# Performance work log

Hardware: AMD Instinct MI355X
Metric: run time of the kernel (lower is better)

## Reference

```python
import jax, jax.numpy as jnp
import numpy as np

B, IN_CH, OFF_CH, OUT_CH, H, W, K = 2, 256, 256, 256, 128, 128, 3
KK = K * K


def setup_inputs() -> dict:
    key = jax.random.key(0)
    k0, k1, k2, k3, k4 = jax.random.split(key, 5)
    x = jax.random.normal(k0, (B, IN_CH, H, W), jnp.float32)
    off = jax.random.normal(k1, (B, OFF_CH, H, W), jnp.float32)
    # xavier_uniform-scale (approximated with scaled normals)
    s_off = (2.0 / (OFF_CH + 3 * KK)) ** 0.5
    w_off = jax.random.normal(k2, (3 * KK, OFF_CH, 1, 1), jnp.float32) * s_off
    b_off = jnp.zeros((3 * KK,), jnp.float32)  # init_offset zeros the bias
    s_w = (2.0 / (IN_CH * KK + OUT_CH * KK)) ** 0.5
    w = jax.random.normal(k3, (OUT_CH, IN_CH, K, K), jnp.float32) * s_w
    b = jax.random.normal(k4, (OUT_CH,), jnp.float32) * 0.01
    return {"x": x, "off": off, "w_off": w_off, "b_off": b_off, "w": w, "b": b}


def _bilinear_gather(x, ys, xs):
    # Zero outside the image (per DCNv2 corner validity check).
    Bb, C, Hin, Win = x.shape
    x_flat = x.reshape(Bb, C, Hin * Win)
    y0 = jnp.floor(ys)
    x0 = jnp.floor(xs)
    wy1 = ys - y0
    wx1 = xs - x0
    wy0 = 1.0 - wy1
    wx0 = 1.0 - wx1

    def corner(yc, xc, wgt):
        valid = (yc >= 0) & (yc <= Hin - 1) & (xc >= 0) & (xc <= Win - 1)
        yi = jnp.clip(yc, 0, Hin - 1).astype(jnp.int32)
        xi = jnp.clip(xc, 0, Win - 1).astype(jnp.int32)
        idx = (yi * Win + xi)[:, None, :]  # [B,1,N]
        v = jnp.take_along_axis(x_flat, idx, axis=2)  # [B,C,N]
        return v * (wgt * valid.astype(x.dtype))[:, None, :]

    return (corner(y0, x0, wy0 * wx0) + corner(y0, x0 + 1, wy0 * wx1)
            + corner(y0 + 1, x0, wy1 * wx0) + corner(y0 + 1, x0 + 1, wy1 * wx1))


def reference(x, off, w_off, b_off, w, b):
    Bb, Cin, Hin, Win = x.shape
    pad = K // 2
    # 1x1 offset/mask conv
    out = jnp.einsum('oc,bchw->bohw', w_off[:, :, 0, 0], off) + b_off[None, :, None, None]
    o1, o2, mask = jnp.split(out, 3, axis=1)
    offset = jnp.concatenate([o1, o2], axis=1)  # [B, 2*KK, H, W]
    mask = jax.nn.sigmoid(mask)                 # [B, KK, H, W]
    # DCNv2 reads offset channels interleaved: (dy_k, dx_k) for kernel point k
    offs = offset.reshape(Bb, KK, 2, Hin, Win)
    dy, dx = offs[:, :, 0], offs[:, :, 1]       # [B, KK, H, W]
    kh = (jnp.arange(KK) // K).astype(x.dtype)
    kw = (jnp.arange(KK) % K).astype(x.dtype)
    iy = jnp.arange(Hin, dtype=x.dtype)
    ix = jnp.arange(Win, dtype=x.dtype)
    ys = iy[None, None, :, None] + (kh - pad)[None, :, None, None] + dy
    xs = ix[None, None, None, :] + (kw - pad)[None, :, None, None] + dx
    val = _bilinear_gather(x, ys.reshape(Bb, -1), xs.reshape(Bb, -1))  # [B,C,KK*H*W]
    val = val.reshape(Bb, Cin, KK, Hin, Win) * mask[:, None]
    y = jnp.einsum('ock,bckhw->bohw', w.reshape(w.shape[0], Cin, KK), val)
    y = y + b[None, :, None, None]
    return jax.nn.relu(y)
```

## Files before the change

### kernel.cpp

```cpp
#include <hip/hip_runtime.h>
#include <stdint.h>

#define HH 128
#define WW 128
#define CIN 256
#define OCH 256
#define HW (HH*WW)

typedef __attribute__((ext_vector_type(8))) short bf16x8;
typedef __attribute__((ext_vector_type(16))) float f32x16;

static __device__ __forceinline__ uint16_t f2bf(float f) {
  uint32_t u = __builtin_bit_cast(uint32_t, f);
  u += 0x7FFFu + ((u >> 16) & 1u);
  return (uint16_t)(u >> 16);
}
static __device__ __forceinline__ float bf2f(uint16_t h) {
  uint32_t u = ((uint32_t)h) << 16;
  return __builtin_bit_cast(float, u);
}

__global__ void pack_w_kernel(const float* __restrict__ w, uint16_t* __restrict__ wpk) {
  int i = blockIdx.x * 256 + threadIdx.x;
  int ci = i & 7;
  int oc = (i >> 3) & 255;
  int c8 = (i >> 11) & 31;
  int k  = i >> 16;
  int c = c8 * 8 + ci;
  wpk[i] = f2bf(w[(oc * 256 + c) * 9 + k]);
}

__global__ void transpose_kernel(const float* __restrict__ x, uint32_t* __restrict__ xt) {
  __shared__ float tile[64][65];
  int wg = blockIdx.x;
  int b  = wg >> 10;
  int r  = wg & 1023;
  int pt = r >> 2, ct = r & 3;
  int p0 = pt * 64, c0 = ct * 64;
  int t = threadIdx.x;
#pragma unroll
  for (int i = 0; i < 16; ++i) {
    int cl = i * 4 + (t >> 6);
    tile[cl][t & 63] = x[(size_t)(b * CIN + c0 + cl) * HW + p0 + (t & 63)];
  }
  __syncthreads();
  int c2 = t & 31, pr = t >> 5;
#pragma unroll
  for (int i = 0; i < 8; ++i) {
    int pl = i * 8 + pr;
    uint32_t lo = f2bf(tile[2 * c2][pl]);
    uint32_t hi = f2bf(tile[2 * c2 + 1][pl]);
    xt[(size_t)(b * HW + p0 + pl) * 128 + (c0 >> 1) + c2] = lo | (hi << 16);
  }
}

__global__ void offc_kernel(const float* __restrict__ off, const float* __restrict__ w_off,
                            const float* __restrict__ b_off, float* __restrict__ offs) {
  __shared__ float wl[27 * 256];
  int t = threadIdx.x;
  for (int r = t; r < 27 * 256; r += 64) wl[r] = w_off[r];
  __syncthreads();
  int px = blockIdx.x * 64 + t;
  int b = px >> 14, yx = px & 16383;
  float acc[27];
#pragma unroll
  for (int j = 0; j < 27; ++j) acc[j] = b_off[j];
  const float* op = off + (size_t)b * CIN * HW + yx;
  for (int c = 0; c < 256; c += 4) {
    float v0 = op[(size_t)(c + 0) * HW];
    float v1 = op[(size_t)(c + 1) * HW];
    float v2 = op[(size_t)(c + 2) * HW];
    float v3 = op[(size_t)(c + 3) * HW];
#pragma unroll
    for (int j = 0; j < 27; ++j) {
      acc[j] = fmaf(wl[j * 256 + c + 0], v0, acc[j]);
      acc[j] = fmaf(wl[j * 256 + c + 1], v1, acc[j]);
      acc[j] = fmaf(wl[j * 256 + c + 2], v2, acc[j]);
      acc[j] = fmaf(wl[j * 256 + c + 3], v3, acc[j]);
    }
  }
  float* o = offs + (size_t)px * 27;
#pragma unroll
  for (int k = 0; k < 9; ++k) {
    o[k * 3 + 0] = acc[2 * k];
    o[k * 3 + 1] = acc[2 * k + 1];
    o[k * 3 + 2] = 1.f / (1.f + expf(-acc[18 + k]));
  }
}

__global__ __launch_bounds__(256) void main_kernel(
    const uint32_t* __restrict__ xt, const float* __restrict__ offs,
    const uint16_t* __restrict__ wpk, const float* __restrict__ bias,
    float* __restrict__ out) {
  __shared__ struct __align__(16) { unsigned char A[64 * 512]; float offs_l[64 * 27]; } sm;

  int wg = blockIdx.x;
  wg = (wg & 7) * 64 + (wg >> 3);
  int b = wg >> 8;
  int tile = wg & 255;
  int y0 = (tile >> 3) * 4, x0 = (tile & 7) * 16;

  int tid = threadIdx.x;
  int lane = tid & 63;
  int wv = tid >> 6;
  int l31 = lane & 31, g = lane >> 5;

  {
    int base = b * HW + y0 * WW + x0;
    for (int r = tid; r < 64 * 27; r += 256) {
      int pyl = r / 432;
      int rem = r - pyl * 432;
      sm.offs_l[pyl * 432 + rem] = offs[(size_t)(base + pyl * WW) * 27 + rem];
    }
  }
  f32x16 acc[2][2] = {};
  __syncthreads();

  const int hw = tid >> 5;
  const int j = tid & 31;
  const uint4* xt4 = (const uint4*)xt;
  const uint4* wp4 = (const uint4*)wpk;
  const int pb = b * HW;
  const uint32_t rswz = (uint32_t)((lane & 7) << 4);

#pragma unroll 1
  for (int k = 0; k < 9; ++k) {
    int kh = k / 3 - 1, kw = k % 3 - 1;
#pragma unroll 2
    for (int i = 0; i < 8; ++i) {
      int px = hw * 8 + i;
      int py = px >> 4, pxx = px & 15;
      float dy = sm.offs_l[px * 27 + k * 3 + 0];
      float dx = sm.offs_l[px * 27 + k * 3 + 1];
      float m  = sm.offs_l[px * 27 + k * 3 + 2];
      float ys = (float)(y0 + py + kh) + dy;
      float xs = (float)(x0 + pxx + kw) + dx;
      float yf = floorf(ys), xf = floorf(xs);
      float wy1 = ys - yf, wx1 = xs - xf;
      float wy0 = 1.f - wy1, wx0 = 1.f - wx1;
      int iy0 = (int)yf, ix0 = (int)xf;
      int iy1 = iy0 + 1, ix1 = ix0 + 1;
      float vy0 = (iy0 >= 0 && iy0 < HH) ? 1.f : 0.f;
      float vy1 = (iy1 >= 0 && iy1 < HH) ? 1.f : 0.f;
      float vx0 = (ix0 >= 0 && ix0 < WW) ? 1.f : 0.f;
      float vx1 = (ix1 >= 0 && ix1 < WW) ? 1.f : 0.f;
      float w00 = wy0 * wx0 * vy0 * vx0 * m;
      float w01 = wy0 * wx1 * vy0 * vx1 * m;
      float w10 = wy1 * wx0 * vy1 * vx0 * m;
      float w11 = wy1 * wx1 * vy1 * vx1 * m;
      int cy0 = iy0 < 0 ? 0 : (iy0 > HH - 1 ? HH - 1 : iy0);
      int cy1 = iy1 < 0 ? 0 : (iy1 > HH - 1 ? HH - 1 : iy1);
      int cx0 = ix0 < 0 ? 0 : (ix0 > WW - 1 ? WW - 1 : ix0);
      int cx1 = ix1 < 0 ? 0 : (ix1 > WW - 1 ? WW - 1 : ix1);
      uint4 q00 = xt4[(size_t)(pb + cy0 * WW + cx0) * 32 + j];
      uint4 q01 = xt4[(size_t)(pb + cy0 * WW + cx1) * 32 + j];
      uint4 q10 = xt4[(size_t)(pb + cy1 * WW + cx0) * 32 + j];
      uint4 q11 = xt4[(size_t)(pb + cy1 * WW + cx1) * 32 + j];
      uint32_t u00[4] = {q00.x, q00.y, q00.z, q00.w};
      uint32_t u01[4] = {q01.x, q01.y, q01.z, q01.w};
      uint32_t u10[4] = {q10.x, q10.y, q10.z, q10.w};
      uint32_t u11[4] = {q11.x, q11.y, q11.z, q11.w};
      uint32_t ow[4];
#pragma unroll
      for (int q = 0; q < 4; ++q) {
        float lo = w00 * bf2f((uint16_t)u00[q]) + w01 * bf2f((uint16_t)u01[q])
                 + w10 * bf2f((uint16_t)u10[q]) + w11 * bf2f((uint16_t)u11[q]);
        float hi = w00 * bf2f((uint16_t)(u00[q] >> 16)) + w01 * bf2f((uint16_t)(u01[q] >> 16))
                 + w10 * bf2f((uint16_t)(u10[q] >> 16)) + w11 * bf2f((uint16_t)(u11[q] >> 16));
        ow[q] = (uint32_t)f2bf(lo) | ((uint32_t)f2bf(hi) << 16);
      }
      *(uint4*)(&sm.A[px * 512 + ((j * 16) ^ ((px & 7) << 4))]) =
          make_uint4(ow[0], ow[1], ow[2], ow[3]);
    }
    __syncthreads();

    int oc0 = wv * 64 + l31;
#pragma unroll
    for (int chunk = 0; chunk < 8; ++chunk) {
#pragma unroll
      for (int cs = 0; cs < 2; ++cs) {
        int boff = (chunk * 64 + cs * 32 + g * 16) ^ rswz;
        uint4 ua0 = *(const uint4*)(&sm.A[l31 * 512 + boff]);
        uint4 ua1 = *(const uint4*)(&sm.A[(l31 + 32) * 512 + boff]);
        int bidx = k * 8192 + (chunk * 4 + cs * 2 + g) * 256;
        uint4 ub0 = wp4[bidx + oc0];
        uint4 ub1 = wp4[bidx + oc0 + 32];
        bf16x8 a0 = __builtin_bit_cast(bf16x8, ua0);
        bf16x8 a1 = __builtin_bit_cast(bf16x8, ua1);
        bf16x8 b0 = __builtin_bit_cast(bf16x8, ub0);
        bf16x8 b1 = __builtin_bit_cast(bf16x8, ub1);
        acc[0][0] = __builtin_amdgcn_mfma_f32_32x32x16_bf16(a0, b0, acc[0][0], 0, 0, 0);
        acc[0][1] = __builtin_amdgcn_mfma_f32_32x32x16_bf16(a0, b1, acc[0][1], 0, 0, 0);
        acc[1][0] = __builtin_amdgcn_mfma_f32_32x32x16_bf16(a1, b0, acc[1][0], 0, 0, 0);
        acc[1][1] = __builtin_amdgcn_mfma_f32_32x32x16_bf16(a1, b1, acc[1][1], 0, 0, 0);
      }
    }
    __syncthreads();
  }

  float bias0 = bias[wv * 64 + l31];
  float bias1 = bias[wv * 64 + 32 + l31];
#pragma unroll
  for (int tm = 0; tm < 2; ++tm) {
#pragma unroll
    for (int tn = 0; tn < 2; ++tn) {
      int oc = wv * 64 + tn * 32 + l31;
      float bv = tn ? bias1 : bias0;
#pragma unroll
      for (int r = 0; r < 16; ++r) {
        int row = (r & 3) + 8 * (r >> 2) + 4 * g + 32 * tm;
        int y = y0 + (row >> 4), x = x0 + (row & 15);
        float v = acc[tm][tn][r] + bv;
        out[((size_t)(b * OCH + oc) << 14) + (y << 7) + x] = fmaxf(v, 0.f);
      }
    }
  }
}

extern "C" void kernel_launch(void* const* d_in, const int* in_sizes, int n_in,
                              void* d_out, int out_size, void* d_ws, size_t ws_size,
                              hipStream_t stream) {
  const float* x     = (const float*)d_in[0];
  const float* off   = (const float*)d_in[1];
  const float* w_off = (const float*)d_in[2];
  const float* b_off = (const float*)d_in[3];
  const float* w     = (const float*)d_in[4];
  const float* bias  = (const float*)d_in[5];
  float* out = (float*)d_out;
  char* ws = (char*)d_ws;
  uint32_t* xt   = (uint32_t*)ws;
  float*    offs = (float*)(ws + 16777216);
  uint16_t* wpk  = (uint16_t*)(ws + 16777216 + 3538944);

  pack_w_kernel<<<2304, 256, 0, stream>>>(w, wpk);
  transpose_kernel<<<2048, 256, 0, stream>>>(x, xt);
  offc_kernel<<<512, 64, 0, stream>>>(off, w_off, b_off, offs);
  main_kernel<<<512, 256, 0, stream>>>(xt, offs, wpk, bias, out);
}
```

Baseline: 262.5 us.

## Double-buffer deformable gather with MFMA, shrink tiles, split offset conv channels

The main kernel now uses 32-pixel tiles with double-buffered LDS. Bilinear gathers for the next kernel tap are issued while MFMAs for the current tap run, using setprio and a single lightweight barrier per tap. The offset conv splits its channel reduction across four waves and reduces through LDS with coalesced output writes, and the transpose uses float4 loads. Smaller tiles double the grid and raise occupancy but halve reuse of the weight (B) operand, which now must be re-read from global per tile.

```diff
diff --git a/kernel.cpp b/kernel.cpp
--- a/kernel.cpp
+++ b/kernel.cpp
@@ -19,6 +19,8 @@
   uint32_t u = ((uint32_t)h) << 16;
   return __builtin_bit_cast(float, u);
 }
+
+#define LBAR() asm volatile("s_waitcnt lgkmcnt(0)\ns_barrier" ::: "memory")
 
 __global__ void pack_w_kernel(const float* __restrict__ w, uint16_t* __restrict__ wpk) {
   int i = blockIdx.x * 256 + threadIdx.x;
@@ -38,10 +40,13 @@
   int pt = r >> 2, ct = r & 3;
   int p0 = pt * 64, c0 = ct * 64;
   int t = threadIdx.x;
-#pragma unroll
-  for (int i = 0; i < 16; ++i) {
-    int cl = i * 4 + (t >> 6);
-    tile[cl][t & 63] = x[(size_t)(b * CIN + c0 + cl) * HW + p0 + (t & 63)];
+  int px4 = (t & 15) * 4;
+#pragma unroll
+  for (int i = 0; i < 4; ++i) {
+    int cl = i * 16 + (t >> 4);
+    const float4 v = *(const float4*)&x[(size_t)(b * CIN + c0 + cl) * HW + p0 + px4];
+    tile[cl][px4 + 0] = v.x; tile[cl][px4 + 1] = v.y;
+    tile[cl][px4 + 2] = v.z; tile[cl][px4 + 3] = v.w;
   }
   __syncthreads();
   int c2 = t & 31, pr = t >> 5;
@@ -54,51 +59,75 @@
   }
 }
 
-__global__ void offc_kernel(const float* __restrict__ off, const float* __restrict__ w_off,
-                            const float* __restrict__ b_off, float* __restrict__ offs) {
+__global__ __launch_bounds__(256) void offc_kernel(const float* __restrict__ off,
+                                                   const float* __restrict__ w_off,
+                                                   const float* __restrict__ b_off,
+                                                   float* __restrict__ offs) {
   __shared__ float wl[27 * 256];
+  __shared__ float red[3][64][29];
   int t = threadIdx.x;
-  for (int r = t; r < 27 * 256; r += 64) wl[r] = w_off[r];
-  __syncthreads();
-  int px = blockIdx.x * 64 + t;
+  for (int r = t; r < 27 * 256; r += 256) wl[r] = w_off[r];
+  int pxl = t & 63, q = t >> 6;
+  int px = blockIdx.x * 64 + pxl;
   int b = px >> 14, yx = px & 16383;
   float acc[27];
 #pragma unroll
-  for (int j = 0; j < 27; ++j) acc[j] = b_off[j];
+  for (int jj = 0; jj < 27; ++jj) acc[jj] = 0.f;
   const float* op = off + (size_t)b * CIN * HW + yx;
-  for (int c = 0; c < 256; c += 4) {
-    float v0 = op[(size_t)(c + 0) * HW];
-    float v1 = op[(size_t)(c + 1) * HW];
-    float v2 = op[(size_t)(c + 2) * HW];
-    float v3 = op[(size_t)(c + 3) * HW];
-#pragma unroll
-    for (int j = 0; j < 27; ++j) {
-      acc[j] = fmaf(wl[j * 256 + c + 0], v0, acc[j]);
-      acc[j] = fmaf(wl[j * 256 + c + 1], v1, acc[j]);
-      acc[j] = fmaf(wl[j * 256 + c + 2], v2, acc[j]);
-      acc[j] = fmaf(wl[j * 256 + c + 3], v3, acc[j]);
-    }
-  }
-  float* o = offs + (size_t)px * 27;
-#pragma unroll
-  for (int k = 0; k < 9; ++k) {
-    o[k * 3 + 0] = acc[2 * k];
-    o[k * 3 + 1] = acc[2 * k + 1];
-    o[k * 3 + 2] = 1.f / (1.f + expf(-acc[18 + k]));
-  }
-}
-
-__global__ __launch_bounds__(256) void main_kernel(
+  int cbase = q * 64;
+  __syncthreads();
+  for (int c = 0; c < 64; c += 4) {
+    float v0 = op[(size_t)(cbase + c + 0) * HW];
+    float v1 = op[(size_t)(cbase + c + 1) * HW];
+    float v2 = op[(size_t)(cbase + c + 2) * HW];
+    float v3 = op[(size_t)(cbase + c + 3) * HW];
+    const float* wr = wl + cbase + c;
+#pragma unroll
+    for (int jj = 0; jj < 27; ++jj) {
+      acc[jj] = fmaf(wr[jj * 256 + 0], v0, acc[jj]);
+      acc[jj] = fmaf(wr[jj * 256 + 1], v1, acc[jj]);
+      acc[jj] = fmaf(wr[jj * 256 + 2], v2, acc[jj]);
+      acc[jj] = fmaf(wr[jj * 256 + 3], v3, acc[jj]);
+    }
+  }
+  if (q > 0) {
+#pragma unroll
+    for (int jj = 0; jj < 27; ++jj) red[q - 1][pxl][jj] = acc[jj];
+  }
+  __syncthreads();
+  if (q == 0) {
+    float fin[27];
+#pragma unroll
+    for (int jj = 0; jj < 27; ++jj)
+      acc[jj] += b_off[jj] + red[0][pxl][jj] + red[1][pxl][jj] + red[2][pxl][jj];
+#pragma unroll
+    for (int k = 0; k < 9; ++k) {
+      fin[3 * k + 0] = acc[2 * k];
+      fin[3 * k + 1] = acc[2 * k + 1];
+      fin[3 * k + 2] = 1.f / (1.f + __expf(-acc[18 + k]));
+    }
+#pragma unroll
+    for (int jj = 0; jj < 27; ++jj) red[0][pxl][jj] = fin[jj];
+  }
+  __syncthreads();
+  float* obase = offs + (size_t)blockIdx.x * 64 * 27;
+  for (int r = t; r < 64 * 27; r += 256) {
+    int p = r / 27, e = r - p * 27;
+    obase[r] = red[0][p][e];
+  }
+}
+
+__global__ __launch_bounds__(256, 4) void main_kernel(
     const uint32_t* __restrict__ xt, const float* __restrict__ offs,
     const uint16_t* __restrict__ wpk, const float* __restrict__ bias,
     float* __restrict__ out) {
-  __shared__ struct __align__(16) { unsigned char A[64 * 512]; float offs_l[64 * 27]; } sm;
+  __shared__ struct __align__(16) { unsigned char A[2][32 * 512]; float offs_l[32 * 27]; } sm;
 
   int wg = blockIdx.x;
-  wg = (wg & 7) * 64 + (wg >> 3);
-  int b = wg >> 8;
-  int tile = wg & 255;
-  int y0 = (tile >> 3) * 4, x0 = (tile & 7) * 16;
+  wg = (wg & 7) * 128 + (wg >> 3);
+  int b = wg >> 9;
+  int tile = wg & 511;
+  int y0 = (tile >> 4) * 4, x0 = (tile & 15) * 8;
 
   int tid = threadIdx.x;
   int lane = tid & 63;
@@ -107,112 +136,141 @@
 
   {
     int base = b * HW + y0 * WW + x0;
-    for (int r = tid; r < 64 * 27; r += 256) {
-      int pyl = r / 432;
-      int rem = r - pyl * 432;
-      sm.offs_l[pyl * 432 + rem] = offs[(size_t)(base + pyl * WW) * 27 + rem];
-    }
-  }
-  f32x16 acc[2][2] = {};
-  __syncthreads();
+    for (int r = tid; r < 32 * 27; r += 256) {
+      int pyl = r / 216;
+      int rem = r - pyl * 216;
+      sm.offs_l[r] = offs[(size_t)(base + pyl * WW) * 27 + rem];
+    }
+  }
+  f32x16 acc[2] = {};
 
   const int hw = tid >> 5;
   const int j = tid & 31;
   const uint4* xt4 = (const uint4*)xt;
   const uint4* wp4 = (const uint4*)wpk;
   const int pb = b * HW;
-  const uint32_t rswz = (uint32_t)((lane & 7) << 4);
+  const uint32_t rswz = (uint32_t)(l31 << 4);
+  const int oc0 = wv * 64 + l31;
+
+  auto issue = [&](int kk, int i, float* wt, uint4* q) {
+    int px = hw * 4 + i;
+    int kh = kk / 3 - 1, kw = kk % 3 - 1;
+    float dy = sm.offs_l[px * 27 + kk * 3 + 0];
+    float dx = sm.offs_l[px * 27 + kk * 3 + 1];
+    float m  = sm.offs_l[px * 27 + kk * 3 + 2];
+    float ys = (float)(y0 + (px >> 3) + kh) + dy;
+    float xs = (float)(x0 + (px & 7) + kw) + dx;
+    float yf = floorf(ys), xf = floorf(xs);
+    float wy1 = ys - yf, wx1 = xs - xf;
+    float wy0 = 1.f - wy1, wx0 = 1.f - wx1;
+    int iy0 = (int)yf, ix0 = (int)xf;
+    int iy1 = iy0 + 1, ix1 = ix0 + 1;
+    float vy0 = (iy0 >= 0 && iy0 < HH) ? 1.f : 0.f;
+    float vy1 = (iy1 >= 0 && iy1 < HH) ? 1.f : 0.f;
+    float vx0 = (ix0 >= 0 && ix0 < WW) ? 1.f : 0.f;
+    float vx1 = (ix1 >= 0 && ix1 < WW) ? 1.f : 0.f;
+    wt[0] = wy0 * wx0 * vy0 * vx0 * m;
+    wt[1] = wy0 * wx1 * vy0 * vx1 * m;
+    wt[2] = wy1 * wx0 * vy1 * vx0 * m;
+    wt[3] = wy1 * wx1 * vy1 * vx1 * m;
+    int cy0 = iy0 < 0 ? 0 : (iy0 > HH - 1 ? HH - 1 : iy0);
+    int cy1 = iy1 < 0 ? 0 : (iy1 > HH - 1 ? HH - 1 : iy1);
+    int cx0 = ix0 < 0 ? 0 : (ix0 > WW - 1 ? WW - 1 : ix0);
+    int cx1 = ix1 < 0 ? 0 : (ix1 > WW - 1 ? WW - 1 : ix1);
+    q[0] = xt4[(size_t)(pb + cy0 * WW + cx0) * 32 + j];
+    q[1] = xt4[(size_t)(pb + cy0 * WW + cx1) * 32 + j];
+    q[2] = xt4[(size_t)(pb + cy1 * WW + cx0) * 32 + j];
+    q[3] = xt4[(size_t)(pb + cy1 * WW + cx1) * 32 + j];
+  };
+
+  auto commit = [&](int i, const float* wt, const uint4* q, int buf) {
+    int px = hw * 4 + i;
+    uint32_t u0[4] = {q[0].x, q[0].y, q[0].z, q[0].w};
+    uint32_t u1[4] = {q[1].x, q[1].y, q[1].z, q[1].w};
+    uint32_t u2[4] = {q[2].x, q[2].y, q[2].z, q[2].w};
+    uint32_t u3[4] = {q[3].x, q[3].y, q[3].z, q[3].w};
+    uint32_t ow[4];
+#pragma unroll
+    for (int qd = 0; qd < 4; ++qd) {
+      float lo = wt[0] * bf2f((uint16_t)u0[qd]) + wt[1] * bf2f((uint16_t)u1[qd])
+               + wt[2] * bf2f((uint16_t)u2[qd]) + wt[3] * bf2f((uint16_t)u3[qd]);
+      float hi = wt[0] * bf2f((uint16_t)(u0[qd] >> 16)) + wt[1] * bf2f((uint16_t)(u1[qd] >> 16))
+               + wt[2] * bf2f((uint16_t)(u2[qd] >> 16)) + wt[3] * bf2f((uint16_t)(u3[qd] >> 16));
+      ow[qd] = (uint32_t)f2bf(lo) | ((uint32_t)f2bf(hi) << 16);
+    }
+    *(uint4*)(&sm.A[buf][px * 512 + ((j * 16) ^ (px << 4))]) =
+        make_uint4(ow[0], ow[1], ow[2], ow[3]);
+  };
+
+  auto mfma_half = [&](int kk, int h, int buf) {
+    __builtin_amdgcn_s_setprio(1);
+#pragma unroll
+    for (int chunk = 0; chunk < 4; ++chunk) {
+#pragma unroll
+      for (int cs = 0; cs < 2; ++cs) {
+        int ch = h * 4 + chunk;
+        int boff = (ch * 64 + cs * 32 + g * 16) ^ rswz;
+        uint4 ua = *(const uint4*)(&sm.A[buf][l31 * 512 + boff]);
+        int bidx = kk * 8192 + (ch * 4 + cs * 2 + g) * 256;
+        uint4 ub0 = wp4[bidx + oc0];
+        uint4 ub1 = wp4[bidx + oc0 + 32];
+        bf16x8 a  = __builtin_bit_cast(bf16x8, ua);
+        bf16x8 b0 = __builtin_bit_cast(bf16x8, ub0);
+        bf16x8 b1 = __builtin_bit_cast(bf16x8, ub1);
+        acc[0] = __builtin_amdgcn_mfma_f32_32x32x16_bf16(a, b0, acc[0], 0, 0, 0);
+        acc[1] = __builtin_amdgcn_mfma_f32_32x32x16_bf16(a, b1, acc[1], 0, 0, 0);
+      }
+    }
+    __builtin_amdgcn_s_setprio(0);
+  };
+
+  LBAR();
+
+  {
+    float wt0[4], wt1[4];
+    uint4 q0[4], q1[4];
+#pragma unroll
+    for (int ip = 0; ip < 2; ++ip) {
+      issue(0, 2 * ip + 0, wt0, q0);
+      issue(0, 2 * ip + 1, wt1, q1);
+      commit(2 * ip + 0, wt0, q0, 0);
+      commit(2 * ip + 1, wt1, q1, 0);
+    }
+  }
 
 #pragma unroll 1
   for (int k = 0; k < 9; ++k) {
-    int kh = k / 3 - 1, kw = k % 3 - 1;
-#pragma unroll 2
-    for (int i = 0; i < 8; ++i) {
-      int px = hw * 8 + i;
-      int py = px >> 4, pxx = px & 15;
-      float dy = sm.offs_l[px * 27 + k * 3 + 0];
-      float dx = sm.offs_l[px * 27 + k * 3 + 1];
-      float m  = sm.offs_l[px * 27 + k * 3 + 2];
-      float ys = (float)(y0 + py + kh) + dy;
-      float xs = (float)(x0 + pxx + kw) + dx;
-      float yf = floorf(ys), xf = floorf(xs);
-      float wy1 = ys - yf, wx1 = xs - xf;
-      float wy0 = 1.f - wy1, wx0 = 1.f - wx1;
-      int iy0 = (int)yf, ix0 = (int)xf;
-      int iy1 = iy0 + 1, ix1 = ix0 + 1;
-      float vy0 = (iy0 >= 0 && iy0 < HH) ? 1.f : 0.f;
-      float vy1 = (iy1 >= 0 && iy1 < HH) ? 1.f : 0.f;
-      float vx0 = (ix0 >= 0 && ix0 < WW) ? 1.f : 0.f;
-      float vx1 = (ix1 >= 0 && ix1 < WW) ? 1.f : 0.f;
-      float w00 = wy0 * wx0 * vy0 * vx0 * m;
-      float w01 = wy0 * wx1 * vy0 * vx1 * m;
-      float w10 = wy1 * wx0 * vy1 * vx0 * m;
-      float w11 = wy1 * wx1 * vy1 * vx1 * m;
-      int cy0 = iy0 < 0 ? 0 : (iy0 > HH - 1 ? HH - 1 : iy0);
-      int cy1 = iy1 < 0 ? 0 : (iy1 > HH - 1 ? HH - 1 : iy1);
-      int cx0 = ix0 < 0 ? 0 : (ix0 > WW - 1 ? WW - 1 : ix0);
-      int cx1 = ix1 < 0 ? 0 : (ix1 > WW - 1 ? WW - 1 : ix1);
-      uint4 q00 = xt4[(size_t)(pb + cy0 * WW + cx0) * 32 + j];
-      uint4 q01 = xt4[(size_t)(pb + cy0 * WW + cx1) * 32 + j];
-      uint4 q10 = xt4[(size_t)(pb + cy1 * WW + cx0) * 32 + j];
-      uint4 q11 = xt4[(size_t)(pb + cy1 * WW + cx1) * 32 + j];
-      uint32_t u00[4] = {q00.x, q00.y, q00.z, q00.w};
-      uint32_t u01[4] = {q01.x, q01.y, q01.z, q01.w};
-      uint32_t u10[4] = {q10.x, q10.y, q10.z, q10.w};
-      uint32_t u11[4] = {q11.x, q11.y, q11.z, q11.w};
-      uint32_t ow[4];
-#pragma unroll
-      for (int q = 0; q < 4; ++q) {
-        float lo = w00 * bf2f((uint16_t)u00[q]) + w01 * bf2f((uint16_t)u01[q])
-                 + w10 * bf2f((uint16_t)u10[q]) + w11 * bf2f((uint16_t)u11[q]);
-        float hi = w00 * bf2f((uint16_t)(u00[q] >> 16)) + w01 * bf2f((uint16_t)(u01[q] >> 16))
-                 + w10 * bf2f((uint16_t)(u10[q] >> 16)) + w11 * bf2f((uint16_t)(u11[q] >> 16));
-        ow[q] = (uint32_t)f2bf(lo) | ((uint32_t)f2bf(hi) << 16);
-      }
-      *(uint4*)(&sm.A[px * 512 + ((j * 16) ^ ((px & 7) << 4))]) =
-          make_uint4(ow[0], ow[1], ow[2], ow[3]);
-    }
-    __syncthreads();
-
-    int oc0 = wv * 64 + l31;
-#pragma unroll
-    for (int chunk = 0; chunk < 8; ++chunk) {
-#pragma unroll
-      for (int cs = 0; cs < 2; ++cs) {
-        int boff = (chunk * 64 + cs * 32 + g * 16) ^ rswz;
-        uint4 ua0 = *(const uint4*)(&sm.A[l31 * 512 + boff]);
-        uint4 ua1 = *(const uint4*)(&sm.A[(l31 + 32) * 512 + boff]);
-        int bidx = k * 8192 + (chunk * 4 + cs * 2 + g) * 256;
-        uint4 ub0 = wp4[bidx + oc0];
-        uint4 ub1 = wp4[bidx + oc0 + 32];
-        bf16x8 a0 = __builtin_bit_cast(bf16x8, ua0);
-        bf16x8 a1 = __builtin_bit_cast(bf16x8, ua1);
-        bf16x8 b0 = __builtin_bit_cast(bf16x8, ub0);
-        bf16x8 b1 = __builtin_bit_cast(bf16x8, ub1);
-        acc[0][0] = __builtin_amdgcn_mfma_f32_32x32x16_bf16(a0, b0, acc[0][0], 0, 0, 0);
-        acc[0][1] = __builtin_amdgcn_mfma_f32_32x32x16_bf16(a0, b1, acc[0][1], 0, 0, 0);
-        acc[1][0] = __builtin_amdgcn_mfma_f32_32x32x16_bf16(a1, b0, acc[1][0], 0, 0, 0);
-        acc[1][1] = __builtin_amdgcn_mfma_f32_32x32x16_bf16(a1, b1, acc[1][1], 0, 0, 0);
-      }
-    }
-    __syncthreads();
-  }
-
-  float bias0 = bias[wv * 64 + l31];
-  float bias1 = bias[wv * 64 + 32 + l31];
-#pragma unroll
-  for (int tm = 0; tm < 2; ++tm) {
-#pragma unroll
-    for (int tn = 0; tn < 2; ++tn) {
-      int oc = wv * 64 + tn * 32 + l31;
-      float bv = tn ? bias1 : bias0;
-#pragma unroll
-      for (int r = 0; r < 16; ++r) {
-        int row = (r & 3) + 8 * (r >> 2) + 4 * g + 32 * tm;
-        int y = y0 + (row >> 4), x = x0 + (row & 15);
-        float v = acc[tm][tn][r] + bv;
-        out[((size_t)(b * OCH + oc) << 14) + (y << 7) + x] = fmaxf(v, 0.f);
-      }
+    int buf = k & 1, nbuf = buf ^ 1;
+    float wt0[4], wt1[4];
+    uint4 q0[4], q1[4];
+    if (k < 8) { issue(k + 1, 0, wt0, q0); issue(k + 1, 1, wt1, q1); }
+    LBAR();
+    mfma_half(k, 0, buf);
+    if (k < 8) {
+      commit(0, wt0, q0, nbuf);
+      commit(1, wt1, q1, nbuf);
+      issue(k + 1, 2, wt0, q0);
+      issue(k + 1, 3, wt1, q1);
+    }
+    mfma_half(k, 1, buf);
+    if (k < 8) {
+      commit(2, wt0, q0, nbuf);
+      commit(3, wt1, q1, nbuf);
+    }
+  }
+
+  float bv0 = bias[wv * 64 + l31];
+  float bv1 = bias[wv * 64 + 32 + l31];
+#pragma unroll
+  for (int tn = 0; tn < 2; ++tn) {
+    int oc = wv * 64 + tn * 32 + l31;
+    float bv = tn ? bv1 : bv0;
+#pragma unroll
+    for (int r = 0; r < 16; ++r) {
+      int row = (r & 3) + 8 * (r >> 2) + 4 * g;
+      int y = y0 + (row >> 3), x = x0 + (row & 7);
+      float v = acc[tn][r] + bv;
+      out[((size_t)(b * OCH + oc) << 14) + (y << 7) + x] = fmaxf(v, 0.f);
     }
   }
 }
@@ -234,6 +292,6 @@
 
   pack_w_kernel<<<2304, 256, 0, stream>>>(w, wpk);
   transpose_kernel<<<2048, 256, 0, stream>>>(x, xt);
-  offc_kernel<<<512, 64, 0, stream>>>(off, w_off, b_off, offs);
-  main_kernel<<<512, 256, 0, stream>>>(xt, offs, wpk, bias, out);
-}
+  offc_kernel<<<512, 256, 0, stream>>>(off, w_off, b_off, offs);
+  main_kernel<<<1024, 256, 0, stream>>>(xt, offs, wpk, bias, out);
+}
```

New measurement: 301.2 us. +14.8%, slower.
